# Kernel tuning notes

Measured on AMD Instinct MI355X. Metric: run time of the kernel, lower is better.

## Reference

```python
import math
import jax
import jax.numpy as jnp
import numpy as np

N_ATOMS = 5000
N_EDGES = 100000
FEAT = 128
BERN_K = 16
R_CUT = 5.0
EPS = 1e-15


def _swish(x, a, b):
    # learnable swish: alpha * x * sigmoid(beta * x)
    return a * x * jax.nn.sigmoid(b * x)


def _y_all(r_ij, r, l):
    """Real spherical harmonics of the unit vector r_ij/r, all m in [-l, l]."""
    x, y, z = r_ij[:, 0], r_ij[:, 1], r_ij[:, 2]
    if l == 0:
        return jnp.ones((r_ij.shape[0], 1), r_ij.dtype)
    if l == 1:
        return jnp.stack([y, z, x], axis=1) / r
    s3 = math.sqrt(3.0)
    r2 = (r * r)[:, 0]
    return jnp.stack(
        [s3 * x * y, s3 * y * z, 1.5 * z * z - 0.5 * r2, s3 * x * z, 0.5 * s3 * (x * x - y * y)],
        axis=1,
    ) / r2[:, None]


def _rho_k(r, gamma, K):
    """Bernstein radial basis b_{k,K-1}(exp(-gamma r)) times SpookyNet smooth cutoff."""
    rr = r[:, 0]
    g = jnp.maximum(gamma, 0.0)  # gamma.clamp(0)
    e = jnp.exp(-g * rr)[:, None]  # [E,1]
    k = jnp.arange(K)
    binom = jnp.asarray([math.comb(K - 1, i) for i in range(K)], dtype=r.dtype)
    bern = binom * e ** k * (1.0 - e) ** (K - 1 - k)  # [E,K]
    safe = jnp.where(rr < R_CUT, (R_CUT - rr) * (R_CUT + rr), 1.0)
    fcut = jnp.where(rr < R_CUT, jnp.exp(-rr * rr / safe), 0.0)
    return bern * fcut[:, None]


def _forward(xyz, x_tilde, rm_W1, rm_b1, rm_W2, rm_b2, rm_W3, rm_b3,
             rl_W1, rl_b1, rl_W2, rl_b2, rl_W3, rl_b3,
             G_s, G_p, G_d, P_1, P_2, D_1, D_2,
             gamma_s, gamma_p, gamma_d, sw_alpha, sw_beta, nbrs):
    n = xyz.shape[0]
    sw = lambda t, i: _swish(t, sw_alpha[i], sw_beta[i])
    # batched pre-activation linear over channel dim c
    bl = lambda W, b, t: jnp.einsum('cij,cnj->cni', W, t) + b[:, None, :]

    # BatchedResidualMLP on x_tilde repeated over 4 channels
    x4 = jnp.broadcast_to(x_tilde, (4,) + x_tilde.shape)  # [4,N,F]
    h = x4 + bl(rm_W2, rm_b2, sw(bl(rm_W1, rm_b1, sw(x4, 0)), 1))
    res_outs = x4 + bl(rm_W3, rm_b3, sw(h, 2))  # [4,N,F]

    i0, i1 = nbrs[:, 0], nbrs[:, 1]
    r_ij = xyz[i1] - xyz[i0]  # [E,3]
    r = jnp.sqrt((r_ij ** 2 + EPS).sum(-1, keepdims=True))  # stable norm, [E,1]
    K = G_s.shape[1]

    def quant(l, gamma, G, res_out):
        # g: [E,K,2l+1] = rho_k outer y_lm
        g = _rho_k(r, gamma, K)[:, :, None] * _y_all(r_ij, r, l)[:, None, :]
        mm = jnp.einsum('fk,ekm->efm', G, g)  # [E,F,2l+1]
        per = res_out[i1][:, :, None] * mm
        return jax.ops.segment_sum(per, i0, num_segments=n)  # scatter_add -> [N,F,2l+1]

    q_s = quant(0, gamma_s, G_s, res_outs[1])
    q_p = quant(1, gamma_p, G_p, res_outs[2])
    q_d = quant(2, gamma_d, G_d, res_outs[3])

    def inner(q, M1, M2):
        t1 = jnp.einsum('ij,njm->nim', M1, q)
        t2 = jnp.einsum('ij,njm->nim', M2, q)
        return (t1 * t2).sum(-1)

    inp = res_outs[0] + q_s[:, :, 0] + inner(q_p, P_1, P_2) + inner(q_d, D_1, D_2)

    # ResidualMLP (note: no outer skip, matching the torch code)
    lin = lambda W, b, t: t @ W.T + b
    h2 = inp + lin(rl_W2, rl_b2, sw(lin(rl_W1, rl_b1, sw(inp, 3)), 4))
    return lin(rl_W3, rl_b3, sw(h2, 5))


def setup_inputs():
    key = jax.random.key(0)
    ks = jax.random.split(key, 24)
    p = lambda k, shape: jax.random.normal(k, shape, dtype=jnp.float32) * 0.1
    F, K = FEAT, BERN_K
    return {
        'xyz': jax.random.normal(ks[0], (N_ATOMS, 3), jnp.float32) * 3.0,
        'x_tilde': jax.random.normal(ks[1], (N_ATOMS, F), jnp.float32),
        'nbrs': jax.random.randint(ks[2], (N_EDGES, 2), 0, N_ATOMS),
        'rm_W1': p(ks[3], (4, F, F)), 'rm_b1': p(ks[4], (4, F)),
        'rm_W2': p(ks[5], (4, F, F)), 'rm_b2': p(ks[6], (4, F)),
        'rm_W3': p(ks[7], (4, F, F)), 'rm_b3': p(ks[8], (4, F)),
        'rl_W1': p(ks[9], (F, F)), 'rl_b1': p(ks[10], (F,)),
        'rl_W2': p(ks[11], (F, F)), 'rl_b2': p(ks[12], (F,)),
        'rl_W3': p(ks[13], (F, F)), 'rl_b3': p(ks[14], (F,)),
        'G_s': p(ks[15], (F, K)), 'G_p': p(ks[16], (F, K)), 'G_d': p(ks[17], (F, K)),
        'P_1': p(ks[18], (F, F)), 'P_2': p(ks[19], (F, F)),
        'D_1': p(ks[20], (F, F)), 'D_2': p(ks[21], (F, F)),
        'gamma_s': jnp.asarray(0.5, jnp.float32),
        'gamma_p': jnp.asarray(0.5, jnp.float32),
        'gamma_d': jnp.asarray(0.5, jnp.float32),
        'sw_alpha': jnp.ones((6,), jnp.float32),
        'sw_beta': jnp.full((6,), 1.702, jnp.float32),
    }


def reference(xyz, x_tilde, nbrs, rm_W1, rm_b1, rm_W2, rm_b2, rm_W3, rm_b3,
              rl_W1, rl_b1, rl_W2, rl_b2, rl_W3, rl_b3,
              G_s, G_p, G_d, P_1, P_2, D_1, D_2,
              gamma_s, gamma_p, gamma_d, sw_alpha, sw_beta):
    return _forward(xyz, x_tilde, rm_W1, rm_b1, rm_W2, rm_b2, rm_W3, rm_b3,
                    rl_W1, rl_b1, rl_W2, rl_b2, rl_W3, rl_b3,
                    G_s, G_p, G_d, P_1, P_2, D_1, D_2,
                    gamma_s, gamma_p, gamma_d, sw_alpha, sw_beta, nbrs)
```

## Files before the change

### kernel.cpp

```cpp
#include <hip/hip_runtime.h>
#include <hip/hip_bf16.h>
#include <math.h>

#define NA 5000
#define NE 100000
#define F 128
#define KB 16
#define RCUT 5.0f
#define RECW 28
#define QCAP 40

typedef long long i64;
typedef __attribute__((ext_vector_type(8))) short bf16x8;
typedef __attribute__((ext_vector_type(4))) float f32x4;

__device__ __forceinline__ float swish_f(float t, float a, float b){
    return a * t / (1.0f + __expf(-b * t));
}
__device__ __forceinline__ float bf2f(unsigned short u){
    return __uint_as_float(((unsigned)u) << 16);
}
__device__ __forceinline__ unsigned short f2bf(float x){
    unsigned b = __float_as_uint(x);
    return (unsigned short)((b + 0x8000u) >> 16);
}
__device__ __forceinline__ unsigned pack2(float a, float b){
    return (unsigned)f2bf(a) | ((unsigned)f2bf(b) << 16);
}
__device__ __forceinline__ int swz(int row, int byte_in_row){
    return row * 256 + (byte_in_row ^ ((row & 7) << 4));
}

template<int MT>
__device__ __forceinline__ void gemm_stage(const unsigned short* __restrict__ Wb,
                                           const short* act_lds, f32x4 (&acc)[MT][2],
                                           int lane, int wave)
{
    bf16x8 B[2][4], A[MT][4];
    const int cl = lane & 15, kh = lane >> 4;
    #pragma unroll
    for (int ntl = 0; ntl < 2; ++ntl){
        const unsigned short* wp = Wb + (i64)(wave * 32 + ntl * 16 + cl) * F + kh * 8;
        #pragma unroll
        for (int kb = 0; kb < 4; ++kb)
            B[ntl][kb] = *(const bf16x8*)(wp + kb * 32);
    }
    #pragma unroll
    for (int mt = 0; mt < MT; ++mt){
        int row = mt * 16 + cl;
        #pragma unroll
        for (int kb = 0; kb < 4; ++kb)
            A[mt][kb] = *(const bf16x8*)((const char*)act_lds + swz(row, kb * 64 + kh * 16));
    }
    #pragma unroll
    for (int mt = 0; mt < MT; ++mt)
        #pragma unroll
        for (int ntl = 0; ntl < 2; ++ntl)
            #pragma unroll
            for (int kb = 0; kb < 4; ++kb)
                acc[mt][ntl] = __builtin_amdgcn_mfma_f32_16x16x32_bf16(
                    A[mt][kb], B[ntl][kb], acc[mt][ntl], 0, 0, 0);
}

__device__ __forceinline__ void epi_lds(f32x4 acc[2][2], const float* __restrict__ bc,
                                        const float* resid_lds, int use_resid,
                                        float aS, float bS, short* act_lds,
                                        int lane, int wave)
{
    const int cl = lane & 15, r4 = (lane >> 4) * 4;
    #pragma unroll
    for (int ntl = 0; ntl < 2; ++ntl){
        int col = wave * 32 + ntl * 16 + cl;
        float bv = bc[col];
        #pragma unroll
        for (int mt = 0; mt < 2; ++mt){
            #pragma unroll
            for (int j = 0; j < 4; ++j){
                int row = mt * 16 + r4 + j;
                float z = acc[mt][ntl][j] + bv;
                if (use_resid) z += resid_lds[row * 132 + col];
                z = swish_f(z, aS, bS);
                *(short*)((char*)act_lds + swz(row, col * 2)) = (short)f2bf(z);
            }
        }
    }
}

__device__ __forceinline__ void basis16(float r, float g, float fcut, float* b){
    const float C[KB] = {1.f,15.f,105.f,455.f,1365.f,3003.f,5005.f,6435.f,
                         6435.f,5005.f,3003.f,1365.f,455.f,105.f,15.f,1.f};
    float e = __expf(-fmaxf(g, 0.f) * r);
    float one = 1.f - e;
    float ep = 1.f;
    #pragma unroll
    for (int k = 0; k < KB; ++k){ b[k] = C[k] * ep * fcut; ep *= e; }
    float op = 1.f;
    #pragma unroll
    for (int k = KB-1; k >= 0; --k){ b[k] *= op; op *= one; }
}

__device__ __forceinline__ void prep_edge_block(
    int ebid, const float* __restrict__ xyz, const int* __restrict__ nbrs,
    int* __restrict__ fill, int* __restrict__ idx,
    const float* __restrict__ gs, const float* __restrict__ gp,
    const float* __restrict__ gd, float* __restrict__ rec)
{
    int e = ebid * 256 + threadIdx.x;
    if (e >= NE) return;
    int i0 = nbrs[2*e], i1 = nbrs[2*e+1];
    float dx = xyz[3*i1]   - xyz[3*i0];
    float dy = xyz[3*i1+1] - xyz[3*i0+1];
    float dz = xyz[3*i1+2] - xyz[3*i0+2];
    float r2 = dx*dx + dy*dy + dz*dz + 3e-15f;
    float r = sqrtf(r2);
    if (r >= RCUT) return;
    int slot = atomicAdd(&fill[i0], 1);
    if (slot < QCAP) idx[i0 * QCAP + slot] = e;
    float* R = rec + (i64)e * RECW;
    float ir = 1.f / r;
    R[0] = __int_as_float(i1);
    R[1] = dx * ir; R[2] = dy * ir; R[3] = dz * ir;
    float fcut = __expf(-r2 / ((RCUT - r) * (RCUT + r)));
    float bs[KB], bp[KB], bd[KB];
    basis16(r, gs[0], fcut, bs);
    basis16(r, gp[0], fcut, bp);
    basis16(r, gd[0], fcut, bd);
    unsigned* RW = (unsigned*)(R + 4);
    #pragma unroll
    for (int k = 0; k < 8; ++k) RW[k]      = pack2(bs[2*k], bs[2*k+1]);
    #pragma unroll
    for (int k = 0; k < 8; ++k) RW[8 + k]  = pack2(bp[2*k], bp[2*k+1]);
    #pragma unroll
    for (int k = 0; k < 8; ++k) RW[16 + k] = pack2(bd[2*k], bd[2*k+1]);
}

template<int S0, int S1, int S2, int ADD2, int ADD3, int ADDPART, int PREP, int CH, int RESB>
__global__ __launch_bounds__(256)
void mlp3_mfma(const float* __restrict__ in, const unsigned short* __restrict__ part,
               const unsigned short* __restrict__ W1b, const float* __restrict__ b1,
               const unsigned short* __restrict__ W2b, const float* __restrict__ b2,
               const unsigned short* __restrict__ W3b, const float* __restrict__ b3,
               float* __restrict__ out, unsigned short* __restrict__ resb,
               const float* __restrict__ sw_a, const float* __restrict__ sw_b, int n,
               const float* __restrict__ xyz, const int* __restrict__ nbrs,
               int* __restrict__ fill, int* __restrict__ idx,
               const float* __restrict__ gs, const float* __restrict__ gp,
               const float* __restrict__ gd, float* __restrict__ rec)
{
    if (PREP && blockIdx.y >= CH){
        int ebid = (blockIdx.y - CH) * gridDim.x + blockIdx.x;
        if (ebid < (NE + 255) / 256)
            prep_edge_block(ebid, xyz, nbrs, fill, idx, gs, gp, gd, rec);
        return;
    }

    __shared__ short act_lds[32 * 128];
    __shared__ float resid_lds[32 * 132];
    const int tid = threadIdx.x;
    const int lane = tid & 63, wave = tid >> 6;
    const int c = blockIdx.y;
    const int a0 = blockIdx.x * 32;
    const i64 S = (i64)NA * F;

    const unsigned short* Wc1 = W1b + (i64)c * F * F;
    const unsigned short* Wc2 = W2b + (i64)c * F * F;
    const unsigned short* Wc3 = W3b + (i64)c * F * F;
    const float* bc1 = b1 + c * F;
    const float* bc2 = b2 + c * F;
    const float* bc3 = b3 + c * F;

    {
        float aS = sw_a[S0], bS = sw_b[S0];
        #pragma unroll
        for (int it = 0; it < 4; ++it){
            int ch = tid + it * 256;
            int row = ch >> 5, j4 = ch & 31;
            int g = a0 + row;
            float4 v = make_float4(0.f, 0.f, 0.f, 0.f);
            if (g < n){
                v = *(const float4*)(in + (i64)g * F + j4 * 4);
                if (ADDPART){
                    #pragma unroll
                    for (int m = 0; m < 8; ++m){
                        ushort4 u = *(const ushort4*)(part + (i64)m * S + (i64)g * F + j4 * 4);
                        v.x += bf2f(u.x); v.y += bf2f(u.y);
                        v.z += bf2f(u.z); v.w += bf2f(u.w);
                    }
                }
            }
            *(float4*)&resid_lds[row * 132 + j4 * 4] = v;
            uint2 p;
            p.x = pack2(swish_f(v.x, aS, bS), swish_f(v.y, aS, bS));
            p.y = pack2(swish_f(v.z, aS, bS), swish_f(v.w, aS, bS));
            *(uint2*)((char*)act_lds + swz(row, j4 * 8)) = p;
        }
    }
    __syncthreads();

    f32x4 acc[2][2];
    #pragma unroll
    for (int a = 0; a < 2; ++a){ acc[a][0] = (f32x4){0,0,0,0}; acc[a][1] = (f32x4){0,0,0,0}; }
    gemm_stage<2>(Wc1, act_lds, acc, lane, wave);
    __syncthreads();
    epi_lds(acc, bc1, resid_lds, 0, sw_a[S1], sw_b[S1], act_lds, lane, wave);
    __syncthreads();

    #pragma unroll
    for (int a = 0; a < 2; ++a){ acc[a][0] = (f32x4){0,0,0,0}; acc[a][1] = (f32x4){0,0,0,0}; }
    gemm_stage<2>(Wc2, act_lds, acc, lane, wave);
    __syncthreads();
    epi_lds(acc, bc2, resid_lds, ADD2, sw_a[S2], sw_b[S2], act_lds, lane, wave);
    __syncthreads();

    #pragma unroll
    for (int a = 0; a < 2; ++a){ acc[a][0] = (f32x4){0,0,0,0}; acc[a][1] = (f32x4){0,0,0,0}; }
    gemm_stage<2>(Wc3, act_lds, acc, lane, wave);
    {
        const int cl = lane & 15, r4 = (lane >> 4) * 4;
        #pragma unroll
        for (int ntl = 0; ntl < 2; ++ntl){
            int col = wave * 32 + ntl * 16 + cl;
            float bv = bc3[col];
            #pragma unroll
            for (int mt = 0; mt < 2; ++mt){
                #pragma unroll
                for (int j = 0; j < 4; ++j){
                    int row = mt * 16 + r4 + j;
                    int g = a0 + row;
                    if (g >= n) continue;
                    float z = acc[mt][ntl][j] + bv;
                    if (ADD3) z += resid_lds[row * 132 + col];
                    if (RESB && c > 0)
                        resb[(i64)(c - 1) * S + (i64)g * F + col] = f2bf(z);
                    else
                        out[(i64)g * F + col] = z;
                }
            }
        }
    }
}

__global__ __launch_bounds__(256)
void bilinear_mfma(const unsigned short* __restrict__ Q,
                   const unsigned short* __restrict__ P1b, const unsigned short* __restrict__ P2b,
                   const unsigned short* __restrict__ D1b, const unsigned short* __restrict__ D2b,
                   unsigned short* __restrict__ part, int n)
{
    __shared__ short act_lds[32 * 128];
    const int tid = threadIdx.x;
    const int lane = tid & 63, wave = tid >> 6;
    const int m = blockIdx.y;
    const int a0 = blockIdx.x * 32;
    const i64 S = (i64)NA * F;
    const unsigned short* M1 = (m < 3) ? P1b : D1b;
    const unsigned short* M2 = (m < 3) ? P2b : D2b;
    const unsigned short* A = Q + (i64)m * S;

    #pragma unroll
    for (int it = 0; it < 2; ++it){
        int ch = tid + it * 256;
        int row = ch >> 4, o16 = ch & 15;
        int g = a0 + row;
        uint4 v = make_uint4(0u, 0u, 0u, 0u);
        if (g < n) v = *(const uint4*)(A + (i64)g * F + o16 * 8);
        *(uint4*)((char*)act_lds + swz(row, o16 * 16)) = v;
    }
    __syncthreads();

    f32x4 acc1[2][2], acc2[2][2];
    #pragma unroll
    for (int a = 0; a < 2; ++a){
        acc1[a][0] = (f32x4){0,0,0,0}; acc1[a][1] = (f32x4){0,0,0,0};
        acc2[a][0] = (f32x4){0,0,0,0}; acc2[a][1] = (f32x4){0,0,0,0};
    }
    gemm_stage<2>(M1, act_lds, acc1, lane, wave);
    gemm_stage<2>(M2, act_lds, acc2, lane, wave);

    const int cl = lane & 15, r4 = (lane >> 4) * 4;
    #pragma unroll
    for (int ntl = 0; ntl < 2; ++ntl){
        int col = wave * 32 + ntl * 16 + cl;
        #pragma unroll
        for (int mt = 0; mt < 2; ++mt){
            #pragma unroll
            for (int j = 0; j < 4; ++j){
                int g = a0 + mt * 16 + r4 + j;
                if (g >= n) continue;
                part[(i64)m * S + (i64)g * F + col] =
                    f2bf(acc1[mt][ntl][j] * acc2[mt][ntl][j]);
            }
        }
    }
}

__global__ __launch_bounds__(256)
void wconv(const float* s0, const float* s1, const float* s2, const float* s3,
           const float* s4, const float* s5, const float* s6, const float* s7,
           const float* s8, const float* s9, const float* g0, const float* g1,
           const float* g2, unsigned short* __restrict__ dst,
           int* __restrict__ fillz)
{
    int t = blockIdx.y;
    if (t == 0){
        for (int i = blockIdx.x * 256 + threadIdx.x; i < NA; i += 32 * 256)
            fillz[i] = 0;
    }
    const float* src; i64 off; int sz;
    if      (t == 0){ src = s0; off = 0;      sz = 65536; }
    else if (t == 1){ src = s1; off = 65536;  sz = 65536; }
    else if (t == 2){ src = s2; off = 131072; sz = 65536; }
    else if (t == 3){ src = s3; off = 196608; sz = 16384; }
    else if (t == 4){ src = s4; off = 212992; sz = 16384; }
    else if (t == 5){ src = s5; off = 229376; sz = 16384; }
    else if (t == 6){ src = s6; off = 245760; sz = 16384; }
    else if (t == 7){ src = s7; off = 262144; sz = 16384; }
    else if (t == 8){ src = s8; off = 278528; sz = 16384; }
    else if (t == 9){ src = s9; off = 294912; sz = 16384; }
    else if (t ==10){ src = g0; off = 311296; sz = 2048; }
    else if (t ==11){ src = g1; off = 313344; sz = 2048; }
    else            { src = g2; off = 315392; sz = 2048; }
    unsigned* d = (unsigned*)(dst + off);
    int pairs = sz >> 1;
    for (int p = blockIdx.x * 256 + threadIdx.x; p < pairs; p += gridDim.x * 256)
        d[p] = pack2(src[2 * p], src[2 * p + 1]);
}

__global__ __launch_bounds__(256)
void q_gather(const float* __restrict__ rec, const int* __restrict__ idx,
              const int* __restrict__ fill,
              const float* __restrict__ res0, const unsigned short* __restrict__ resb,
              const unsigned* __restrict__ Gb,
              float* __restrict__ inp, unsigned short* __restrict__ Q)
{
    const int n = blockIdx.x;
    const int tid = threadIdx.x;
    const int s = tid >> 7;
    const int f = tid & 127;
    const int lane = tid & 63, wave = tid >> 6;
    const i64 S = (i64)NA * F;

    __shared__ int   idx_s[QCAP];
    __shared__ float recs[QCAP * RECW];
    __shared__ __align__(16) char upool[12288];
    unsigned short* D = (unsigned short*)upool;
    float* red = (float*)upool;

    if (tid < QCAP) idx_s[tid] = idx[n * QCAP + tid];
    const int cnt = min(fill[n], QCAP);
    __syncthreads();
    for (int w = tid; w < cnt * RECW; w += 256){
        int j = w / RECW, o = w - j * RECW;
        recs[w] = rec[(i64)idx_s[j] * RECW + o];
    }
    __syncthreads();

    float qs = 0.f;
    float qp0=0.f, qp1=0.f, qp2=0.f;
    float qd0=0.f, qd1=0.f, qd2=0.f, qd3=0.f, qd4=0.f;
    const float s3 = 1.7320508075688772f;
    const int cl = lane & 15, kh = lane >> 4;

    for (int base = 0; base < cnt; base += 16){
        {
            int er = base + cl; if (er >= QCAP) er = 0;
            bf16x8 A[3];
            #pragma unroll
            for (int ch = 0; ch < 3; ++ch){
                if (kh < 2){
                    const unsigned* bw = (const unsigned*)&recs[er * RECW + 4];
                    union { uint4 u; bf16x8 h; } cv;
                    cv.u = *(const uint4*)(bw + ch * 8 + kh * 4);
                    A[ch] = cv.h;
                } else {
                    A[ch] = (bf16x8){0,0,0,0,0,0,0,0};
                }
            }
            #pragma unroll
            for (int ch = 0; ch < 3; ++ch){
                #pragma unroll
                for (int ct = 0; ct < 2; ++ct){
                    int fc = wave * 32 + ct * 16 + cl;
                    bf16x8 B;
                    if (kh < 2){
                        union { uint4 u; bf16x8 h; } cv;
                        cv.u = *(const uint4*)(Gb + (i64)ch * F * 8 + fc * 8 + kh * 4);
                        B = cv.h;
                    } else {
                        B = (bf16x8){0,0,0,0,0,0,0,0};
                    }
                    f32x4 z = (f32x4){0.f, 0.f, 0.f, 0.f};
                    z = __builtin_amdgcn_mfma_f32_16x16x32_bf16(A[ch], B, z, 0, 0, 0);
                    #pragma unroll
                    for (int j = 0; j < 4; ++j)
                        D[ch * 2048 + (kh * 4 + j) * 128 + fc] = f2bf(z[j]);
                }
            }
        }
        __syncthreads();

        const int mrec = min(16, cnt - base);
        int j = s;
        float a1n = 0.f, a2n = 0.f, a3n = 0.f;
        if (j < mrec){
            int i1 = __float_as_int(recs[(base + j) * RECW]);
            a1n = bf2f(resb[(i64)i1 * F + f]);
            a2n = bf2f(resb[S + (i64)i1 * F + f]);
            a3n = bf2f(resb[2 * S + (i64)i1 * F + f]);
        }
        for (; j < mrec; j += 2){
            float a1 = a1n, a2 = a2n, a3 = a3n;
            int jn = j + 2;
            if (jn < mrec){
                int i1 = __float_as_int(recs[(base + jn) * RECW]);
                a1n = bf2f(resb[(i64)i1 * F + f]);
                a2n = bf2f(resb[S + (i64)i1 * F + f]);
                a3n = bf2f(resb[2 * S + (i64)i1 * F + f]);
            }
            const float* R = &recs[(base + j) * RECW];
            float ux = R[1], uy = R[2], uz = R[3];
            float ds = bf2f(D[0 * 2048 + j * 128 + f]);
            float dp = bf2f(D[1 * 2048 + j * 128 + f]);
            float dd = bf2f(D[2 * 2048 + j * 128 + f]);
            qs += a1 * ds;
            float tp = a2 * dp;
            qp0 += tp * uy; qp1 += tp * uz; qp2 += tp * ux;
            float td = a3 * dd;
            qd0 += td * (s3 * ux * uy);
            qd1 += td * (s3 * uy * uz);
            qd2 += td * (1.5f * uz * uz - 0.5f);
            qd3 += td * (s3 * ux * uz);
            qd4 += td * (0.5f * s3 * (ux*ux - uy*uy));
        }
        __syncthreads();
    }

    red[(s * 9 + 0) * 128 + f] = qs;
    red[(s * 9 + 1) * 128 + f] = qp0; red[(s * 9 + 2) * 128 + f] = qp1;
    red[(s * 9 + 3) * 128 + f] = qp2;
    red[(s * 9 + 4) * 128 + f] = qd0; red[(s * 9 + 5) * 128 + f] = qd1;
    red[(s * 9 + 6) * 128 + f] = qd2; red[(s * 9 + 7) * 128 + f] = qd3;
    red[(s * 9 + 8) * 128 + f] = qd4;
    __syncthreads();
    if (s == 0){
        float sums[9];
        #pragma unroll
        for (int i = 0; i < 9; ++i)
            sums[i] = red[(0 * 9 + i) * 128 + f] + red[(1 * 9 + i) * 128 + f];
        inp[(i64)n*F + f] = res0[(i64)n*F + f] + sums[0];
        #pragma unroll
        for (int mm = 0; mm < 8; ++mm)
            Q[(i64)mm * S + (i64)n*F + f] = f2bf(sums[1 + mm]);
    }
}

extern "C" void kernel_launch(void* const* d_in, const int* in_sizes, int n_in,
                              void* d_out, int out_size, void* d_ws, size_t ws_size,
                              hipStream_t stream)
{
    const float* xyz     = (const float*)d_in[0];
    const float* x_tilde = (const float*)d_in[1];
    const int*   nbrs    = (const int*)d_in[2];
    const float* rm_W1 = (const float*)d_in[3],  *rm_b1 = (const float*)d_in[4];
    const float* rm_W2 = (const float*)d_in[5],  *rm_b2 = (const float*)d_in[6];
    const float* rm_W3 = (const float*)d_in[7],  *rm_b3 = (const float*)d_in[8];
    const float* rl_W1 = (const float*)d_in[9],  *rl_b1 = (const float*)d_in[10];
    const float* rl_W2 = (const float*)d_in[11], *rl_b2 = (const float*)d_in[12];
    const float* rl_W3 = (const float*)d_in[13], *rl_b3 = (const float*)d_in[14];
    const float* G_s = (const float*)d_in[15], *G_p = (const float*)d_in[16], *G_d = (const float*)d_in[17];
    const float* P_1 = (const float*)d_in[18], *P_2 = (const float*)d_in[19];
    const float* D_1 = (const float*)d_in[20], *D_2 = (const float*)d_in[21];
    const float* gamma_s = (const float*)d_in[22], *gamma_p = (const float*)d_in[23], *gamma_d = (const float*)d_in[24];
    const float* sw_a = (const float*)d_in[25], *sw_b = (const float*)d_in[26];

    const i64 S = (i64)NA * F;
    float* res0 = (float*)d_ws;
    unsigned short* resb = (unsigned short*)(res0 + S);
    float* inp  = (float*)(resb + 3 * S);
    unsigned short* Q = (unsigned short*)(inp + S);
    float* rec  = (float*)(Q + 8 * S);
    unsigned short* part = (unsigned short*)rec;
    int* fill   = (int*)(rec + (i64)NE * RECW);
    int* idx    = fill + NA + 8;
    unsigned short* Wb = (unsigned short*)(idx + NA * QCAP);

    const int NT = (NA + 31) / 32;

    wconv<<<dim3(32, 13), 256, 0, stream>>>(rm_W1, rm_W2, rm_W3, rl_W1, rl_W2, rl_W3,
                                            P_1, P_2, D_1, D_2, G_s, G_p, G_d, Wb, fill);

    mlp3_mfma<0,1,2,1,1,0,1,4,1><<<dim3(NT, 7), 256, 0, stream>>>(
        x_tilde, (const unsigned short*)nullptr,
        Wb + 0, rm_b1, Wb + 65536, rm_b2, Wb + 131072, rm_b3,
        res0, resb, sw_a, sw_b, NA,
        xyz, nbrs, fill, idx, gamma_s, gamma_p, gamma_d, rec);

    q_gather<<<NA, 256, 0, stream>>>(rec, idx, fill, res0, resb,
                                     (const unsigned*)(Wb + 311296), inp, Q);

    bilinear_mfma<<<dim3(NT, 8), 256, 0, stream>>>(
        Q, Wb + 245760, Wb + 262144, Wb + 278528, Wb + 294912, part, NA);

    mlp3_mfma<3,4,5,1,0,1,0,1,0><<<dim3(NT, 1), 256, 0, stream>>>(
        inp, part,
        Wb + 196608, rl_b1, Wb + 212992, rl_b2, Wb + 229376, rl_b3,
        (float*)d_out, nullptr, sw_a, sw_b, NA,
        nullptr, nullptr, nullptr, nullptr, nullptr, nullptr, nullptr, nullptr);
}
```

Before: 77.53 us.

## Fuse bilinear MFMA products and reduction into q_gather per-atom kernel

Removes the separate bilinear_mfma launch and the bf16 Q and part buffers. Each q_gather block now stages its atom's 8 Q vectors in LDS, padded to 16 rows, and runs the P/D matmuls with MFMA directly. It then reduces the elementwise products across the m rows with shuffles and adds the result into inp, so the final MLP no longer sums 8 partial arrays. The cost is that every block reloads all four 128x128 weight matrices from global/L2 for a single atom and wastes half of each MFMA tile on zero rows.

```diff
diff --git a/kernel.cpp b/kernel.cpp
--- a/kernel.cpp
+++ b/kernel.cpp
@@ -9,6 +9,7 @@
 #define RCUT 5.0f
 #define RECW 28
 #define QCAP 40
+#define QSTR 136
 
 typedef long long i64;
 typedef __attribute__((ext_vector_type(8))) short bf16x8;
@@ -134,9 +135,9 @@
     for (int k = 0; k < 8; ++k) RW[16 + k] = pack2(bd[2*k], bd[2*k+1]);
 }
 
-template<int S0, int S1, int S2, int ADD2, int ADD3, int ADDPART, int PREP, int CH, int RESB>
+template<int S0, int S1, int S2, int ADD2, int ADD3, int PREP, int CH, int RESB>
 __global__ __launch_bounds__(256)
-void mlp3_mfma(const float* __restrict__ in, const unsigned short* __restrict__ part,
+void mlp3_mfma(const float* __restrict__ in,
                const unsigned short* __restrict__ W1b, const float* __restrict__ b1,
                const unsigned short* __restrict__ W2b, const float* __restrict__ b2,
                const unsigned short* __restrict__ W3b, const float* __restrict__ b3,
@@ -177,17 +178,7 @@
             int row = ch >> 5, j4 = ch & 31;
             int g = a0 + row;
             float4 v = make_float4(0.f, 0.f, 0.f, 0.f);
-            if (g < n){
-                v = *(const float4*)(in + (i64)g * F + j4 * 4);
-                if (ADDPART){
-                    #pragma unroll
-                    for (int m = 0; m < 8; ++m){
-                        ushort4 u = *(const ushort4*)(part + (i64)m * S + (i64)g * F + j4 * 4);
-                        v.x += bf2f(u.x); v.y += bf2f(u.y);
-                        v.z += bf2f(u.z); v.w += bf2f(u.w);
-                    }
-                }
-            }
+            if (g < n) v = *(const float4*)(in + (i64)g * F + j4 * 4);
             *(float4*)&resid_lds[row * 132 + j4 * 4] = v;
             uint2 p;
             p.x = pack2(swish_f(v.x, aS, bS), swish_f(v.y, aS, bS));
@@ -235,59 +226,6 @@
                     else
                         out[(i64)g * F + col] = z;
                 }
-            }
-        }
-    }
-}
-
-__global__ __launch_bounds__(256)
-void bilinear_mfma(const unsigned short* __restrict__ Q,
-                   const unsigned short* __restrict__ P1b, const unsigned short* __restrict__ P2b,
-                   const unsigned short* __restrict__ D1b, const unsigned short* __restrict__ D2b,
-                   unsigned short* __restrict__ part, int n)
-{
-    __shared__ short act_lds[32 * 128];
-    const int tid = threadIdx.x;
-    const int lane = tid & 63, wave = tid >> 6;
-    const int m = blockIdx.y;
-    const int a0 = blockIdx.x * 32;
-    const i64 S = (i64)NA * F;
-    const unsigned short* M1 = (m < 3) ? P1b : D1b;
-    const unsigned short* M2 = (m < 3) ? P2b : D2b;
-    const unsigned short* A = Q + (i64)m * S;
-
-    #pragma unroll
-    for (int it = 0; it < 2; ++it){
-        int ch = tid + it * 256;
-        int row = ch >> 4, o16 = ch & 15;
-        int g = a0 + row;
-        uint4 v = make_uint4(0u, 0u, 0u, 0u);
-        if (g < n) v = *(const uint4*)(A + (i64)g * F + o16 * 8);
-        *(uint4*)((char*)act_lds + swz(row, o16 * 16)) = v;
-    }
-    __syncthreads();
-
-    f32x4 acc1[2][2], acc2[2][2];
-    #pragma unroll
-    for (int a = 0; a < 2; ++a){
-        acc1[a][0] = (f32x4){0,0,0,0}; acc1[a][1] = (f32x4){0,0,0,0};
-        acc2[a][0] = (f32x4){0,0,0,0}; acc2[a][1] = (f32x4){0,0,0,0};
-    }
-    gemm_stage<2>(M1, act_lds, acc1, lane, wave);
-    gemm_stage<2>(M2, act_lds, acc2, lane, wave);
-
-    const int cl = lane & 15, r4 = (lane >> 4) * 4;
-    #pragma unroll
-    for (int ntl = 0; ntl < 2; ++ntl){
-        int col = wave * 32 + ntl * 16 + cl;
-        #pragma unroll
-        for (int mt = 0; mt < 2; ++mt){
-            #pragma unroll
-            for (int j = 0; j < 4; ++j){
-                int g = a0 + mt * 16 + r4 + j;
-                if (g >= n) continue;
-                part[(i64)m * S + (i64)g * F + col] =
-                    f2bf(acc1[mt][ntl][j] * acc2[mt][ntl][j]);
             }
         }
     }
@@ -330,7 +268,8 @@
               const int* __restrict__ fill,
               const float* __restrict__ res0, const unsigned short* __restrict__ resb,
               const unsigned* __restrict__ Gb,
-              float* __restrict__ inp, unsigned short* __restrict__ Q)
+              const unsigned short* __restrict__ Wb,
+              float* __restrict__ inp)
 {
     const int n = blockIdx.x;
     const int tid = threadIdx.x;
@@ -342,8 +281,10 @@
     __shared__ int   idx_s[QCAP];
     __shared__ float recs[QCAP * RECW];
     __shared__ __align__(16) char upool[12288];
+    __shared__ float inpbase[128];
     unsigned short* D = (unsigned short*)upool;
     float* red = (float*)upool;
+    unsigned short* Qlds = (unsigned short*)upool;
 
     if (tid < QCAP) idx_s[tid] = idx[n * QCAP + tid];
     const int cnt = min(fill[n], QCAP);
@@ -441,15 +382,76 @@
     red[(s * 9 + 6) * 128 + f] = qd2; red[(s * 9 + 7) * 128 + f] = qd3;
     red[(s * 9 + 8) * 128 + f] = qd4;
     __syncthreads();
+
+    float sums[9];
     if (s == 0){
-        float sums[9];
         #pragma unroll
         for (int i = 0; i < 9; ++i)
             sums[i] = red[(0 * 9 + i) * 128 + f] + red[(1 * 9 + i) * 128 + f];
-        inp[(i64)n*F + f] = res0[(i64)n*F + f] + sums[0];
-        #pragma unroll
-        for (int mm = 0; mm < 8; ++mm)
-            Q[(i64)mm * S + (i64)n*F + f] = f2bf(sums[1 + mm]);
+    }
+    __syncthreads();
+
+    if (s == 0){
+        inpbase[f] = res0[(i64)n * F + f] + sums[0];
+        #pragma unroll
+        for (int m = 0; m < 8; ++m)
+            Qlds[m * QSTR + f] = f2bf(sums[1 + m]);
+    } else {
+        #pragma unroll
+        for (int m = 8; m < 16; ++m)
+            Qlds[m * QSTR + f] = 0;
+    }
+    __syncthreads();
+
+    {
+        bf16x8 A[4];
+        #pragma unroll
+        for (int kb = 0; kb < 4; ++kb)
+            A[kb] = *(const bf16x8*)(Qlds + cl * QSTR + kb * 32 + kh * 8);
+
+        const unsigned short* P1b = Wb + 245760;
+        const unsigned short* P2b = Wb + 262144;
+        const unsigned short* D1b = Wb + 278528;
+        const unsigned short* D2b = Wb + 294912;
+
+        float psum[2];
+        #pragma unroll
+        for (int ct = 0; ct < 2; ++ct){
+            int fc = wave * 32 + ct * 16 + cl;
+            f32x4 aP1 = (f32x4){0,0,0,0}, aP2 = (f32x4){0,0,0,0};
+            f32x4 aD1 = (f32x4){0,0,0,0}, aD2 = (f32x4){0,0,0,0};
+            #pragma unroll
+            for (int kb = 0; kb < 4; ++kb){
+                bf16x8 bP1 = *(const bf16x8*)(P1b + (i64)fc * F + kb * 32 + kh * 8);
+                bf16x8 bP2 = *(const bf16x8*)(P2b + (i64)fc * F + kb * 32 + kh * 8);
+                bf16x8 bD1 = *(const bf16x8*)(D1b + (i64)fc * F + kb * 32 + kh * 8);
+                bf16x8 bD2 = *(const bf16x8*)(D2b + (i64)fc * F + kb * 32 + kh * 8);
+                aP1 = __builtin_amdgcn_mfma_f32_16x16x32_bf16(A[kb], bP1, aP1, 0, 0, 0);
+                aP2 = __builtin_amdgcn_mfma_f32_16x16x32_bf16(A[kb], bP2, aP2, 0, 0, 0);
+                aD1 = __builtin_amdgcn_mfma_f32_16x16x32_bf16(A[kb], bD1, aD1, 0, 0, 0);
+                aD2 = __builtin_amdgcn_mfma_f32_16x16x32_bf16(A[kb], bD2, aD2, 0, 0, 0);
+            }
+            float sum = 0.f;
+            if (kh == 0){
+                sum += aP1[0]*aP2[0] + aP1[1]*aP2[1] + aP1[2]*aP2[2];
+                sum += aD1[3]*aD2[3];
+            } else if (kh == 1){
+                sum += aD1[0]*aD2[0] + aD1[1]*aD2[1] + aD1[2]*aD2[2] + aD1[3]*aD2[3];
+            }
+            psum[ct] = sum;
+        }
+        #pragma unroll
+        for (int ct = 0; ct < 2; ++ct){
+            psum[ct] += __shfl_xor(psum[ct], 16);
+            psum[ct] += __shfl_xor(psum[ct], 32);
+        }
+        if (kh == 0){
+            #pragma unroll
+            for (int ct = 0; ct < 2; ++ct){
+                int fc = wave * 32 + ct * 16 + cl;
+                inp[(i64)n * F + fc] = inpbase[fc] + psum[ct];
+            }
+        }
     }
 }
 
@@ -476,9 +478,7 @@
     float* res0 = (float*)d_ws;
     unsigned short* resb = (unsigned short*)(res0 + S);
     float* inp  = (float*)(resb + 3 * S);
-    unsigned short* Q = (unsigned short*)(inp + S);
-    float* rec  = (float*)(Q + 8 * S);
-    unsigned short* part = (unsigned short*)rec;
+    float* rec  = inp + S;
     int* fill   = (int*)(rec + (i64)NE * RECW);
     int* idx    = fill + NA + 8;
     unsigned short* Wb = (unsigned short*)(idx + NA * QCAP);
@@ -488,20 +488,17 @@
     wconv<<<dim3(32, 13), 256, 0, stream>>>(rm_W1, rm_W2, rm_W3, rl_W1, rl_W2, rl_W3,
                                             P_1, P_2, D_1, D_2, G_s, G_p, G_d, Wb, fill);
 
-    mlp3_mfma<0,1,2,1,1,0,1,4,1><<<dim3(NT, 7), 256, 0, stream>>>(
-        x_tilde, (const unsigned short*)nullptr,
+    mlp3_mfma<0,1,2,1,1,1,4,1><<<dim3(NT, 7), 256, 0, stream>>>(
+        x_tilde,
         Wb + 0, rm_b1, Wb + 65536, rm_b2, Wb + 131072, rm_b3,
         res0, resb, sw_a, sw_b, NA,
         xyz, nbrs, fill, idx, gamma_s, gamma_p, gamma_d, rec);
 
     q_gather<<<NA, 256, 0, stream>>>(rec, idx, fill, res0, resb,
-                                     (const unsigned*)(Wb + 311296), inp, Q);
-
-    bilinear_mfma<<<dim3(NT, 8), 256, 0, stream>>>(
-        Q, Wb + 245760, Wb + 262144, Wb + 278528, Wb + 294912, part, NA);
-
-    mlp3_mfma<3,4,5,1,0,1,0,1,0><<<dim3(NT, 1), 256, 0, stream>>>(
-        inp, part,
+                                     (const unsigned*)(Wb + 311296), Wb, inp);
+
+    mlp3_mfma<3,4,5,1,0,0,1,0><<<dim3(NT, 1), 256, 0, stream>>>(
+        inp,
         Wb + 196608, rl_b1, Wb + 212992, rl_b2, Wb + 229376, rl_b3,
         (float*)d_out, nullptr, sw_a, sw_b, NA,
         nullptr, nullptr, nullptr, nullptr, nullptr, nullptr, nullptr, nullptr);
```

After: 125.2 us. 1.61x slower.
